# Performance work log

Hardware: AMD Instinct MI355X
Metric: run time of the kernel (lower is better)

## Reference

```python
import jax, jax.numpy as jnp
import numpy as np

B, T, DM, H, DK, DV = 2, 2048, 1024, 16, 64, 64


def setup_inputs() -> dict:
    key = jax.random.key(0)
    k = jax.random.split(key, 7)
    std_k = np.float32(1.0 / np.sqrt(DK))
    std_v = np.float32(1.0 / np.sqrt(DV))
    return {
        "xq": jax.random.normal(k[0], (B, T, DM), jnp.float32),
        "xk": jax.random.normal(k[1], (B, T, DM), jnp.float32),
        "xv": jax.random.normal(k[2], (B, T, DM), jnp.float32),
        "mask": jnp.ones((B, T), jnp.float32),  # padding mask: 1 = keep
        "w_q": jax.random.normal(k[3], (H, DM, DK), jnp.float32) * std_k,
        "w_k": jax.random.normal(k[4], (H, DM, DK), jnp.float32) * std_k,
        "w_v": jax.random.normal(k[5], (H, DM, DV), jnp.float32) * std_v,
        "w_o": jax.random.normal(k[6], (H * DV, DM), jnp.float32) * np.float32(1.0 / np.sqrt(H * DV)),
        "b_o": jnp.zeros((DM,), jnp.float32),
    }


def reference(xq, xk, xv, mask, w_q, w_k, w_v, w_o, b_o):
    d_k = w_q.shape[-1]
    # per-head projections: [B,T,DM] x [H,DM,DK] -> [B,H,T,DK]
    q = jnp.einsum('bsd,hdk->bhsk', xq, w_q)
    kk = jnp.einsum('btd,hdk->bhtk', xk, w_k)
    v = jnp.einsum('btd,hdv->bhtv', xv, w_v)
    # NOTE: source divides by d_k (not sqrt(d_k)) -- kept faithful
    scores = jnp.einsum('bhsk,bhtk->bhst', q, kk) / jnp.float32(d_k)
    # _padding_mask: multiply by mask broadcast over key dim, then any exact
    # zero (masked OR coincidentally zero score) becomes -inf -- kept faithful
    masked = scores * mask[:, None, None, :]
    scores = jnp.where(masked == 0.0, -jnp.inf, masked)
    attn = jax.nn.softmax(scores, axis=-1)
    out = jnp.einsum('bhst,bhtv->bhsv', attn, v)  # [B,H,T,DV]
    b, h, t, dv = out.shape
    concat = out.transpose(0, 2, 1, 3).reshape(b, t, h * dv)
    return concat @ w_o + b_o
```

## Files before the change

kernel.cpp:

```cpp
#include <hip/hip_runtime.h>
#include <hip/hip_bf16.h>


typedef __attribute__((ext_vector_type(8))) short short8;
typedef __attribute__((ext_vector_type(4))) short short4v;
typedef __attribute__((ext_vector_type(4))) float f32x4;
typedef __attribute__((ext_vector_type(4))) int i32x4;

__device__ __forceinline__ short f2bf(float f) {
  union { float f; unsigned u; } v; v.f = f;
  unsigned r = v.u + 0x7FFFu + ((v.u >> 16) & 1u);
  return (short)(r >> 16);
}

#define GLD_LDS(g, l) __builtin_amdgcn_global_load_lds( \
    (const __attribute__((address_space(1))) void*)(g), \
    (__attribute__((address_space(3))) void*)(l), 16, 0, 0)

__global__ __launch_bounds__(256) void prep_all(
    const float* __restrict__ xq, const float* __restrict__ xk,
    const float* __restrict__ xv, const float* __restrict__ wq,
    const float* __restrict__ wk, const float* __restrict__ wv,
    const float* __restrict__ wo,
    short* __restrict__ Xb, short* __restrict__ Wall, short* __restrict__ Wot)
{
  const int bx = blockIdx.x, tid = threadIdx.x;
  __shared__ float Lt[64][65];
  if (bx < 6144) {
    int z = bx >> 11;
    const float* x = z == 0 ? xq : (z == 1 ? xk : xv);
    size_t i = ((size_t)(bx & 2047) * 256 + tid) * 8;
    f32x4 f0 = *(const f32x4*)(x + i);
    f32x4 f1 = *(const f32x4*)(x + i + 4);
    short8 s;
#pragma unroll
    for (int j = 0; j < 4; j++) { s[j] = f2bf(f0[j]); s[4 + j] = f2bf(f1[j]); }
    *(short8*)(Xb + (size_t)z * 4194304 + i) = s;
  } else if (bx < 6912) {
    int bz = bx - 6144;
    int z = bz >> 8, inner = bz & 255;
    const float* w = z == 0 ? wq : (z == 1 ? wk : wv);
    short* Wt = Wall + (size_t)z * 1048576;
    int h = inner >> 4, d0 = (inner & 15) * 64;
#pragma unroll
    for (int it = 0; it < 4; it++) {
      int e = tid + it * 256;
      int dl = e >> 4, k4 = (e & 15) * 4;
      f32x4 v = *(const f32x4*)(w + ((size_t)(h * 1024 + d0 + dl) * 64) + k4);
#pragma unroll
      for (int j = 0; j < 4; j++) Lt[dl][k4 + j] = v[j];
    }
    __syncthreads();
#pragma unroll
    for (int it = 0; it < 4; it++) {
      int e = tid + it * 256;
      int kl = e >> 4, dq = e & 15;
      short4v s;
#pragma unroll
      for (int j = 0; j < 4; j++) s[j] = f2bf(Lt[dq * 4 + j][kl]);
      *(short4v*)(Wt + (size_t)(h * 64 + kl) * 1024 + d0 + dq * 4) = s;
    }
  } else {
    int bz = bx - 6912;
    int k0 = (bz >> 4) * 64, n0 = (bz & 15) * 64;
#pragma unroll
    for (int it = 0; it < 4; it++) {
      int e = tid + it * 256;
      int kl = e >> 4, n4 = (e & 15) * 4;
      f32x4 v = *(const f32x4*)(wo + (size_t)(k0 + kl) * 1024 + n0 + n4);
#pragma unroll
      for (int j = 0; j < 4; j++) Lt[kl][n4 + j] = v[j];
    }
    __syncthreads();
#pragma unroll
    for (int it = 0; it < 4; it++) {
      int e = tid + it * 256;
      int nl = e >> 4, kq = e & 15;
      short4v s;
#pragma unroll
      for (int j = 0; j < 4; j++) s[j] = f2bf(Lt[kq * 4 + j][nl]);
      *(short4v*)(Wot + (size_t)(n0 + nl) * 1024 + k0 + kq * 4) = s;
    }
  }
}

__global__ __launch_bounds__(256) void proj_qkv2(
    const short* __restrict__ Xb, const short* __restrict__ Wall,
    short* __restrict__ Qb, short* __restrict__ Kt2, short* __restrict__ Vt2)
{
  const int z = blockIdx.z;
  const short* X  = Xb   + (size_t)z * 4194304;
  const short* Wt = Wall + (size_t)z * 1048576;

  const int t0 = blockIdx.x * 128;
  const int n0 = blockIdx.y * 128;
  const int tid = threadIdx.x, w = tid >> 6, lane = tid & 63;
  const int c = lane & 15, q4 = lane >> 4;
  const int wn = (w & 1) * 64, wt = (w >> 1) * 64;
  const int srow = lane >> 2, scol = (lane & 3) * 8;

  __shared__ __align__(16) short Al[128 * 32];
  __shared__ __align__(16) short Bl[128 * 32];

  f32x4 acc[4][4] = {};

  for (int k0 = 0; k0 < 1024; k0 += 32) {
#pragma unroll
    for (int i = 0; i < 2; i++) {
      int rg = (w * 2 + i) * 16;
      GLD_LDS(Wt + (size_t)(n0 + rg + srow) * 1024 + k0 + scol, Al + rg * 32);
      GLD_LDS(X  + (size_t)(t0 + rg + srow) * 1024 + k0 + scol, Bl + rg * 32);
    }
    __syncthreads();
    short8 a[4], bfr[4];
#pragma unroll
    for (int i = 0; i < 4; i++)
      a[i] = *(const short8*)(Al + (wn + i * 16 + c) * 32 + q4 * 8);
#pragma unroll
    for (int j = 0; j < 4; j++)
      bfr[j] = *(const short8*)(Bl + (wt + j * 16 + c) * 32 + q4 * 8);
#pragma unroll
    for (int i = 0; i < 4; i++)
#pragma unroll
      for (int j = 0; j < 4; j++)
        acc[i][j] = __builtin_amdgcn_mfma_f32_16x16x32_bf16(a[i], bfr[j], acc[i][j], 0, 0, 0);
    __syncthreads();
  }

#pragma unroll
  for (int i = 0; i < 4; i++)
#pragma unroll
    for (int j = 0; j < 4; j++) {
      int n = n0 + wn + i * 16 + q4 * 4;
      int trow = t0 + wt + j * 16 + c;
      int b = trow >> 11, t = trow & 2047;
      int h = n >> 6, cc = n & 63;
      int bh = b * 16 + h;
      f32x4 v = acc[i][j];
      short4v pk;
#pragma unroll
      for (int r = 0; r < 4; r++) pk[r] = f2bf(v[r]);
      if (z == 0) {
        *(short4v*)(Qb + (size_t)(bh * 2048 + t) * 64 + cc) = pk;
      } else if (z == 1) {
        int t5 = t & 31, s_ = t5 >> 4, c_ = t5 & 15;
        size_t base = (size_t)bh * 131072 + (t >> 5) * 2048;
        size_t off = base + ((s_ * 2 + (cc >> 5)) * 16 + c_) * 32 +
                     ((cc >> 3) & 3) * 8 + (cc & 7);
        *(short4v*)(Kt2 + off) = pk;
      } else {
        int t5 = t & 31;
        int kp = ((t5 >> 2) & 3) * 8 + ((t5 >> 4) & 1) * 4 + (t5 & 3);
        size_t base = (size_t)bh * 131072 + (t >> 5) * 2048;
#pragma unroll
        for (int r = 0; r < 4; r++)
          Vt2[base + (size_t)(cc + r) * 32 + kp] = pk[r];
      }
    }
}

__global__ __launch_bounds__(256, 2) void attn9(
    const short* __restrict__ Qb, const short* __restrict__ Kt2,
    const short* __restrict__ Vt2, const float* __restrict__ mask,
    short* __restrict__ AO)
{
  const int bh = blockIdx.x;
  const int tblk = blockIdx.y;
  const int b = bh >> 4, h = bh & 15;
  const short* Qh = Qb  + (size_t)bh * 131072;
  const short* Kh = Kt2 + (size_t)bh * 131072;
  const short* Vh = Vt2 + (size_t)bh * 131072;

  const int tid = threadIdx.x, w = tid >> 6, lane = tid & 63;
  const int c = lane & 15, q4 = lane >> 4;
  const int qrow0 = tblk * 128 + w * 32;

  __shared__ __align__(16) short KV[3][4096];
  __shared__ __align__(16) float cmL[2048];
  __shared__ __align__(16) float cbL[2048];

  const int ch = c * 4 + q4;
  const int rdo = (ch ^ ((ch >> 3) & 3)) * 8;
  const int sch = (lane ^ ((lane >> 3) & 3)) * 8;

  {
    const float LOG2E_64c = 1.44269504088896f * 0.015625f;
    f32x4 m0 = *(const f32x4*)(mask + b * 2048 + tid * 8);
    f32x4 m1 = *(const f32x4*)(mask + b * 2048 + tid * 8 + 4);
    *(f32x4*)(&cmL[tid * 8])     = m0 * LOG2E_64c;
    *(f32x4*)(&cmL[tid * 8 + 4]) = m1 * LOG2E_64c;
    *(f32x4*)(&cbL[tid * 8])     = (m0 - 1.0f) * 240.0f;
    *(f32x4*)(&cbL[tid * 8 + 4]) = (m1 - 1.0f) * 240.0f;
  }

  short8 qa[2][2];
#pragma unroll
  for (int u = 0; u < 2; u++)
#pragma unroll
    for (int dc = 0; dc < 2; dc++)
      qa[u][dc] = *(const short8*)(Qh + (size_t)(qrow0 + u * 16 + c) * 64 + dc * 32 + q4 * 8);

  f32x4 acc[2][4] = {};
  float l[2] = {0.f, 0.f};

  const int g0 = w * 2;

#define STAGE(BI, T) do { \
    const short* sb = (g0 < 4) ? (Kh + (size_t)(T) * 2048 + g0 * 512) \
                               : (Vh + (size_t)(T) * 2048 + (g0 - 4) * 512); \
    GLD_LDS(sb + sch,        &KV[BI][g0 * 512]); \
    GLD_LDS(sb + 512 + sch,  &KV[BI][g0 * 512 + 512]); \
  } while (0)

#define QK(BI, ST, VA) do { \
    const short* Kb = &KV[BI][0]; \
    short8 kf[2][2]; \
    _Pragma("unroll") \
    for (int s = 0; s < 2; s++) \
      _Pragma("unroll") \
      for (int dc = 0; dc < 2; dc++) \
        kf[s][dc] = *(const short8*)(Kb + (s * 2 + dc) * 512 + rdo); \
    _Pragma("unroll") \
    for (int vs = 0; vs < 4; vs++) \
      VA[vs] = *(const short8*)(Kb + (4 + vs) * 512 + rdo); \
    _Pragma("unroll") \
    for (int u = 0; u < 2; u++) \
      _Pragma("unroll") \
      for (int s = 0; s < 2; s++) { \
        f32x4 z = {}; \
        z = __builtin_amdgcn_mfma_f32_16x16x32_bf16(kf[s][0], qa[u][0], z, 0, 0, 0); \
        ST[u][s] = __builtin_amdgcn_mfma_f32_16x16x32_bf16(kf[s][1], qa[u][1], z, 0, 0, 0); \
      } \
  } while (0)

#define SMPV(ST, VA, TT) do { \
    f32x4 cm[2], cb[2]; \
    _Pragma("unroll") \
    for (int s = 0; s < 2; s++) { \
      cm[s] = *(const f32x4*)(&cmL[(TT) * 32 + q4 * 4 + s * 16]); \
      cb[s] = *(const f32x4*)(&cbL[(TT) * 32 + q4 * 4 + s * 16]); \
    } \
    _Pragma("unroll") \
    for (int u = 0; u < 2; u++) { \
      unsigned pkd[2][2]; \
      _Pragma("unroll") \
      for (int s = 0; s < 2; s++) { \
        float e0 = __builtin_amdgcn_exp2f(ST[u][s][0] * cm[s][0] + cb[s][0]); \
        float e1 = __builtin_amdgcn_exp2f(ST[u][s][1] * cm[s][1] + cb[s][1]); \
        float e2 = __builtin_amdgcn_exp2f(ST[u][s][2] * cm[s][2] + cb[s][2]); \
        float e3 = __builtin_amdgcn_exp2f(ST[u][s][3] * cm[s][3] + cb[s][3]); \
        l[u] += (e0 + e1) + (e2 + e3); \
        unsigned p01, p23; \
        asm("v_cvt_pk_bf16_f32 %0, %1, %2" : "=v"(p01) : "v"(e0), "v"(e1)); \
        asm("v_cvt_pk_bf16_f32 %0, %1, %2" : "=v"(p23) : "v"(e2), "v"(e3)); \
        pkd[s][0] = p01; pkd[s][1] = p23; \
      } \
      union { i32x4 i; short8 s; } pb; \
      pb.i[0] = (int)pkd[0][0]; pb.i[1] = (int)pkd[0][1]; \
      pb.i[2] = (int)pkd[1][0]; pb.i[3] = (int)pkd[1][1]; \
      _Pragma("unroll") \
      for (int vs = 0; vs < 4; vs++) \
        acc[u][vs] = __builtin_amdgcn_mfma_f32_16x16x32_bf16(VA[vs], pb.s, acc[u][vs], 0, 0, 0); \
    } \
  } while (0)

  f32x4 stA[2][2], stB[2][2];
  short8 vaA[4], vaB[4];

  __syncthreads();
  asm volatile("s_waitcnt vmcnt(0)" ::: "memory");
  __builtin_amdgcn_sched_barrier(0);
  STAGE(0, 0);
  STAGE(1, 1);
  asm volatile("s_waitcnt vmcnt(2) lgkmcnt(0)" ::: "memory");
  __builtin_amdgcn_sched_barrier(0);
  __builtin_amdgcn_s_barrier();
  __builtin_amdgcn_sched_barrier(0);
  STAGE(2, 2);
  QK(0, stA, vaA);

  int bs = 0;
  for (int ii = 0; ii < 31; ++ii) {
    const int t = 2 * ii;
    asm volatile("s_waitcnt vmcnt(2) lgkmcnt(0)" ::: "memory");
    __builtin_amdgcn_sched_barrier(0);
    __builtin_amdgcn_s_barrier();
    __builtin_amdgcn_sched_barrier(0);
    if (t + 3 < 64) STAGE(bs, t + 3);
    {
      int bn = bs + 1; if (bn == 3) bn = 0;
      QK(bn, stB, vaB);
    }
    SMPV(stA, vaA, t);
    bs = bs + 1; if (bs == 3) bs = 0;
    asm volatile("s_waitcnt vmcnt(2) lgkmcnt(0)" ::: "memory");
    __builtin_amdgcn_sched_barrier(0);
    __builtin_amdgcn_s_barrier();
    __builtin_amdgcn_sched_barrier(0);
    if (t + 4 < 64) STAGE(bs, t + 4);
    {
      int bn = bs + 1; if (bn == 3) bn = 0;
      QK(bn, stA, vaA);
    }
    SMPV(stB, vaB, t + 1);
    bs = bs + 1; if (bs == 3) bs = 0;
  }
  asm volatile("s_waitcnt vmcnt(0) lgkmcnt(0)" ::: "memory");
  __builtin_amdgcn_sched_barrier(0);
  __builtin_amdgcn_s_barrier();
  __builtin_amdgcn_sched_barrier(0);
  QK(0, stB, vaB);
  SMPV(stA, vaA, 62);
  SMPV(stB, vaB, 63);
#undef STAGE
#undef QK
#undef SMPV

#pragma unroll
  for (int u = 0; u < 2; u++) {
    float lu = l[u];
    lu += __shfl_xor(lu, 16);
    lu += __shfl_xor(lu, 32);
    float inv = 1.0f / lu;
    size_t row = (size_t)b * 2048 + qrow0 + u * 16 + c;
#pragma unroll
    for (int vs = 0; vs < 4; vs++) {
      f32x4 v = acc[u][vs];
      short4v pk;
#pragma unroll
      for (int r = 0; r < 4; r++) pk[r] = f2bf(v[r] * inv);
      *(short4v*)(AO + row * 1024 + h * 64 + vs * 16 + q4 * 4) = pk;
    }
  }
}

__global__ __launch_bounds__(256) void out_proj2(
    const short* __restrict__ AO, const short* __restrict__ Wot,
    const float* __restrict__ bo, float* __restrict__ out)
{
  const int t0 = blockIdx.x * 128;
  const int n0 = blockIdx.y * 128;
  const int tid = threadIdx.x, w = tid >> 6, lane = tid & 63;
  const int c = lane & 15, q4 = lane >> 4;
  const int wn = (w & 1) * 64, wt = (w >> 1) * 64;
  const int srow = lane >> 2, scol = (lane & 3) * 8;

  __shared__ __align__(16) short Al[128 * 32];
  __shared__ __align__(16) short Bl[128 * 32];

  f32x4 acc[4][4] = {};

  for (int k0 = 0; k0 < 1024; k0 += 32) {
#pragma unroll
    for (int i = 0; i < 2; i++) {
      int rg = (w * 2 + i) * 16;
      GLD_LDS(Wot + (size_t)(n0 + rg + srow) * 1024 + k0 + scol, Al + rg * 32);
      GLD_LDS(AO  + (size_t)(t0 + rg + srow) * 1024 + k0 + scol, Bl + rg * 32);
    }
    __syncthreads();
    short8 a[4], bfr[4];
#pragma unroll
    for (int i = 0; i < 4; i++)
      a[i] = *(const short8*)(Al + (wn + i * 16 + c) * 32 + q4 * 8);
#pragma unroll
    for (int j = 0; j < 4; j++)
      bfr[j] = *(const short8*)(Bl + (wt + j * 16 + c) * 32 + q4 * 8);
#pragma unroll
    for (int i = 0; i < 4; i++)
#pragma unroll
      for (int j = 0; j < 4; j++)
        acc[i][j] = __builtin_amdgcn_mfma_f32_16x16x32_bf16(a[i], bfr[j], acc[i][j], 0, 0, 0);
    __syncthreads();
  }

#pragma unroll
  for (int i = 0; i < 4; i++)
#pragma unroll
    for (int j = 0; j < 4; j++) {
      int n = n0 + wn + i * 16 + q4 * 4;
      int trow = t0 + wt + j * 16 + c;
      f32x4 v = acc[i][j] + *(const f32x4*)(bo + n);
      *(f32x4*)(out + (size_t)trow * 1024 + n) = v;
    }
}

extern "C" void kernel_launch(void* const* d_in, const int* in_sizes, int n_in,
                              void* d_out, int out_size, void* d_ws, size_t ws_size,
                              hipStream_t stream)
{
  (void)in_sizes; (void)n_in; (void)out_size; (void)ws_size;
  const float* xq   = (const float*)d_in[0];
  const float* xk   = (const float*)d_in[1];
  const float* xv   = (const float*)d_in[2];
  const float* mask = (const float*)d_in[3];
  const float* wq   = (const float*)d_in[4];
  const float* wk   = (const float*)d_in[5];
  const float* wv   = (const float*)d_in[6];
  const float* wo   = (const float*)d_in[7];
  const float* bo   = (const float*)d_in[8];
  float* out = (float*)d_out;

  char* ws = (char*)d_ws;
  short* Wall = (short*)(ws + (size_t)0);
  short* Wot  = (short*)(ws + ((size_t)6 << 20));
  short* Xb   = (short*)(ws + ((size_t)8 << 20));
  short* AO   = (short*)(ws + ((size_t)8 << 20));
  short* Qb   = (short*)(ws + ((size_t)32 << 20));
  short* Kt2  = (short*)(ws + ((size_t)40 << 20));
  short* Vt2  = (short*)(ws + ((size_t)48 << 20));

  prep_all<<<7168, 256, 0, stream>>>(xq, xk, xv, wq, wk, wv, wo, Xb, Wall, Wot);
  proj_qkv2<<<dim3(32, 8, 3), 256, 0, stream>>>(Xb, Wall, Qb, Kt2, Vt2);
  attn9<<<dim3(32, 16), 256, 0, stream>>>(Qb, Kt2, Vt2, mask, AO);
  out_proj2<<<dim3(32, 8), 256, 0, stream>>>(AO, Wot, bo, out);
}
```

Measured before the change: 222.1 us.

## Load V fragments directly from global into registers, stage only K in LDS

Attention kernel now stages only K tiles through LDS via global_load_lds, while V fragments are prefetched straight from global memory into registers two tiles ahead of use. This halves the LDS footprint and LDS read traffic per tile, and changes the waitcnt schedule and the loop peeling to match. In exchange, each wave issues its own V global loads with no sharing across waves, which adds more vmem traffic and register pressure, and the vmcnt bookkeeping becomes more fragile.

```diff
diff --git a/kernel.cpp b/kernel.cpp
--- a/kernel.cpp
+++ b/kernel.cpp
@@ -159,7 +159,7 @@
     }
 }
 
-__global__ __launch_bounds__(256, 2) void attn9(
+__global__ __launch_bounds__(256, 2) void attn13(
     const short* __restrict__ Qb, const short* __restrict__ Kt2,
     const short* __restrict__ Vt2, const float* __restrict__ mask,
     short* __restrict__ AO)
@@ -175,13 +175,14 @@
   const int c = lane & 15, q4 = lane >> 4;
   const int qrow0 = tblk * 128 + w * 32;
 
-  __shared__ __align__(16) short KV[3][4096];
+  __shared__ __align__(16) short Kl[3][2048];
   __shared__ __align__(16) float cmL[2048];
   __shared__ __align__(16) float cbL[2048];
 
   const int ch = c * 4 + q4;
   const int rdo = (ch ^ ((ch >> 3) & 3)) * 8;
   const int sch = (lane ^ ((lane >> 3) & 3)) * 8;
+  const int vch = c * 32 + q4 * 8;
 
   {
     const float LOG2E_64c = 1.44269504088896f * 0.015625f;
@@ -203,26 +204,25 @@
   f32x4 acc[2][4] = {};
   float l[2] = {0.f, 0.f};
 
-  const int g0 = w * 2;
-
-#define STAGE(BI, T) do { \
-    const short* sb = (g0 < 4) ? (Kh + (size_t)(T) * 2048 + g0 * 512) \
-                               : (Vh + (size_t)(T) * 2048 + (g0 - 4) * 512); \
-    GLD_LDS(sb + sch,        &KV[BI][g0 * 512]); \
-    GLD_LDS(sb + 512 + sch,  &KV[BI][g0 * 512 + 512]); \
+#define STAGE(BI, T) \
+    GLD_LDS(Kh + (size_t)(T) * 2048 + w * 512 + sch, &Kl[BI][w * 512])
+
+#define PREFV(VA, T1) do { \
+    const short* vb = Vh + (size_t)(T1) * 2048 + vch; \
+    VA[0] = *(const short8*)(vb); \
+    VA[1] = *(const short8*)(vb + 512); \
+    VA[2] = *(const short8*)(vb + 1024); \
+    VA[3] = *(const short8*)(vb + 1536); \
   } while (0)
 
-#define QK(BI, ST, VA) do { \
-    const short* Kb = &KV[BI][0]; \
+#define QK(BI, ST) do { \
+    const short* Kb = &Kl[BI][0]; \
     short8 kf[2][2]; \
     _Pragma("unroll") \
     for (int s = 0; s < 2; s++) \
       _Pragma("unroll") \
       for (int dc = 0; dc < 2; dc++) \
         kf[s][dc] = *(const short8*)(Kb + (s * 2 + dc) * 512 + rdo); \
-    _Pragma("unroll") \
-    for (int vs = 0; vs < 4; vs++) \
-      VA[vs] = *(const short8*)(Kb + (4 + vs) * 512 + rdo); \
     _Pragma("unroll") \
     for (int u = 0; u < 2; u++) \
       _Pragma("unroll") \
@@ -264,6 +264,12 @@
     } \
   } while (0)
 
+#define WAITVL(N) do { \
+    asm volatile("s_waitcnt vmcnt(" #N ") lgkmcnt(0)" ::: "memory"); \
+    __builtin_amdgcn_sched_barrier(0); } while (0)
+#define SBAR() do { __builtin_amdgcn_s_barrier(); \
+    __builtin_amdgcn_sched_barrier(0); } while (0)
+
   f32x4 stA[2][2], stB[2][2];
   short8 vaA[4], vaB[4];
 
@@ -272,49 +278,55 @@
   __builtin_amdgcn_sched_barrier(0);
   STAGE(0, 0);
   STAGE(1, 1);
-  asm volatile("s_waitcnt vmcnt(2) lgkmcnt(0)" ::: "memory");
-  __builtin_amdgcn_sched_barrier(0);
-  __builtin_amdgcn_s_barrier();
-  __builtin_amdgcn_sched_barrier(0);
+  PREFV(vaA, 0);
+  WAITVL(5);
+  SBAR();
   STAGE(2, 2);
-  QK(0, stA, vaA);
+  QK(0, stA);
+  PREFV(vaB, 1);
 
   int bs = 0;
-  for (int ii = 0; ii < 31; ++ii) {
+  for (int ii = 0; ii < 30; ++ii) {
     const int t = 2 * ii;
-    asm volatile("s_waitcnt vmcnt(2) lgkmcnt(0)" ::: "memory");
-    __builtin_amdgcn_sched_barrier(0);
-    __builtin_amdgcn_s_barrier();
-    __builtin_amdgcn_sched_barrier(0);
-    if (t + 3 < 64) STAGE(bs, t + 3);
-    {
-      int bn = bs + 1; if (bn == 3) bn = 0;
-      QK(bn, stB, vaB);
-    }
+    int b1 = bs + 1; if (b1 == 3) b1 = 0;
+    int b2 = b1 + 1; if (b2 == 3) b2 = 0;
+    WAITVL(5);
+    SBAR();
+    STAGE(bs, t + 3);
+    QK(b1, stB);
     SMPV(stA, vaA, t);
-    bs = bs + 1; if (bs == 3) bs = 0;
-    asm volatile("s_waitcnt vmcnt(2) lgkmcnt(0)" ::: "memory");
-    __builtin_amdgcn_sched_barrier(0);
-    __builtin_amdgcn_s_barrier();
-    __builtin_amdgcn_sched_barrier(0);
-    if (t + 4 < 64) STAGE(bs, t + 4);
-    {
-      int bn = bs + 1; if (bn == 3) bn = 0;
-      QK(bn, stA, vaA);
-    }
+    PREFV(vaA, t + 2);
+    WAITVL(5);
+    SBAR();
+    STAGE(b1, t + 4);
+    QK(b2, stA);
     SMPV(stB, vaB, t + 1);
-    bs = bs + 1; if (bs == 3) bs = 0;
-  }
-  asm volatile("s_waitcnt vmcnt(0) lgkmcnt(0)" ::: "memory");
-  __builtin_amdgcn_sched_barrier(0);
-  __builtin_amdgcn_s_barrier();
-  __builtin_amdgcn_sched_barrier(0);
-  QK(0, stB, vaB);
+    PREFV(vaB, t + 3);
+    bs = b2;
+  }
+  WAITVL(5);
+  SBAR();
+  STAGE(0, 63);
+  QK(1, stB);
+  SMPV(stA, vaA, 60);
+  PREFV(vaA, 62);
+  WAITVL(5);
+  SBAR();
+  QK(2, stA);
+  SMPV(stB, vaB, 61);
+  PREFV(vaB, 63);
+  WAITVL(4);
+  SBAR();
+  QK(0, stB);
   SMPV(stA, vaA, 62);
+  WAITVL(0);
   SMPV(stB, vaB, 63);
 #undef STAGE
+#undef PREFV
 #undef QK
 #undef SMPV
+#undef WAITVL
+#undef SBAR
 
 #pragma unroll
   for (int u = 0; u < 2; u++) {
@@ -411,6 +423,6 @@
 
   prep_all<<<7168, 256, 0, stream>>>(xq, xk, xv, wq, wk, wv, wo, Xb, Wall, Wot);
   proj_qkv2<<<dim3(32, 8, 3), 256, 0, stream>>>(Xb, Wall, Qb, Kt2, Vt2);
-  attn9<<<dim3(32, 16), 256, 0, stream>>>(Qb, Kt2, Vt2, mask, AO);
+  attn13<<<dim3(32, 16), 256, 0, stream>>>(Qb, Kt2, Vt2, mask, AO);
   out_proj2<<<dim3(32, 8), 256, 0, stream>>>(AO, Wot, bo, out);
 }
```

Result: slower. 227.7 us (+2.5%).
